# Optimization experiments

Hardware: AMD Instinct MI355X
Metric: run time of the kernel (lower is better)

## Reference

```python
import jax, jax.numpy as jnp
import numpy as np

N = 100000
E = 3200000
IN_C, HID_C, OUT_C = 128, 64, 16
NEG_SLOPE = 0.2


def setup_inputs() -> dict:
    key = jax.random.key(0)
    ks = jax.random.split(key, 12)
    x = jax.random.normal(ks[0], (N, IN_C), dtype=jnp.float32)
    # edges with no self-loops (reference then appends one self-loop per node,
    # matching add_remaining_self_loops on a loop-free graph)
    src = jax.random.randint(ks[1], (E,), 0, N)
    off = jax.random.randint(ks[2], (E,), 1, N)
    dst = (src + off) % N
    edge_index = jnp.stack([src, dst]).astype(jnp.int64)
    W1 = jax.random.normal(ks[3], (IN_C, HID_C), jnp.float32) / np.sqrt(IN_C)
    a_src1 = jax.random.normal(ks[4], (HID_C,), jnp.float32) / np.sqrt(HID_C)
    a_dst1 = jax.random.normal(ks[5], (HID_C,), jnp.float32) / np.sqrt(HID_C)
    b1 = jnp.zeros((HID_C,), jnp.float32)
    W2 = jax.random.normal(ks[6], (HID_C, OUT_C), jnp.float32) / np.sqrt(HID_C)
    a_src2 = jax.random.normal(ks[7], (OUT_C,), jnp.float32) / np.sqrt(OUT_C)
    a_dst2 = jax.random.normal(ks[8], (OUT_C,), jnp.float32) / np.sqrt(OUT_C)
    b2 = jnp.zeros((OUT_C,), jnp.float32)
    return {"x": x, "edge_index": edge_index, "W1": W1, "a_src1": a_src1,
            "a_dst1": a_dst1, "b1": b1, "W2": W2, "a_src2": a_src2,
            "a_dst2": a_dst2, "b2": b2}


def gat_conv(x, src, dst, W, a_src, a_dst, b):
    # x: [N, Cin] -> h: [N, Cout]
    h = x @ W
    # per-node attention halves, then per-edge score e_ij = LeakyReLU(a_s[src]+a_d[dst])
    s = h @ a_src  # [N]
    d = h @ a_dst  # [N]
    e = jax.nn.leaky_relu(s[src] + d[dst], NEG_SLOPE)  # [E']
    # segment softmax over incoming edges of each destination node
    m = jax.ops.segment_max(e, dst, num_segments=N)
    m = jnp.where(jnp.isfinite(m), m, 0.0)
    p = jnp.exp(e - m[dst])
    z = jax.ops.segment_sum(p, dst, num_segments=N)
    coef = p / (z[dst] + 1e-16)  # [E']
    # scatter-aggregate messages h[src] weighted by attention
    out = jax.ops.segment_sum(coef[:, None] * h[src], dst, num_segments=N)
    return out + b


def reference(x, edge_index, W1, a_src1, a_dst1, b1, W2, a_src2, a_dst2, b2):
    # add_remaining_self_loops: input graph has no self-loops, so append all N
    loop = jnp.arange(N, dtype=edge_index.dtype)
    src = jnp.concatenate([edge_index[0], loop])
    dst = jnp.concatenate([edge_index[1], loop])
    h = gat_conv(x, src, dst, W1, a_src1, a_dst1, b1)
    h = jax.nn.relu(h)  # dropout is identity at eval
    h = gat_conv(h, src, dst, W2, a_src2, a_dst2, b2)
    return jax.nn.log_softmax(h, axis=1)
```

## Files before the change

### kernel.cpp

```cpp
#include <hip/hip_runtime.h>
#include <math.h>

#define NEG 0.2f

__device__ __forceinline__ float leaky(float x){ return x >= 0.f ? x : NEG*x; }

__device__ __forceinline__ unsigned short f2b(float f){
    unsigned u = __float_as_uint(f);
    unsigned r = u + 0x7fffu + ((u >> 16) & 1u);
    return (unsigned short)(r >> 16);
}

__global__ void k_rank(const int* __restrict__ ei, int* __restrict__ cnt,
                       int* __restrict__ rank, int E, int ET){
    int i = blockIdx.x*256 + threadIdx.x;
    if (i >= ET) return;
    int dst = (i < E) ? ei[E + i] : (i - E);
    rank[i] = atomicAdd(&cnt[dst << 4], 1);
}
__global__ void k_scan1(const int* __restrict__ cnt, int* __restrict__ bsum, int n){
    __shared__ int sh[256];
    int b = blockIdx.x, tid = threadIdx.x;
    int start = b*1024, s = 0;
    for (int i = tid; i < 1024; i += 256){ int idx = start+i; s += (idx<n)?cnt[idx<<4]:0; }
    sh[tid]=s; __syncthreads();
    for (int d=128; d>0; d>>=1){ if (tid<d) sh[tid]+=sh[tid+d]; __syncthreads(); }
    if (tid==0) bsum[b]=sh[0];
}
__global__ void k_scan2(int* bsum, int nb){
    if (threadIdx.x==0 && blockIdx.x==0){
        int run=0;
        for (int i=0;i<nb;i++){ int v=bsum[i]; bsum[i]=run; run+=v; }
    }
}
__global__ void k_scan3(const int* __restrict__ cnt, const int* __restrict__ bsum,
                        int* __restrict__ rowptr, int n){
    __shared__ int sh[256];
    int b = blockIdx.x, tid = threadIdx.x;
    int i0 = b*1024 + tid*4;
    int v[4]; int local=0;
    #pragma unroll
    for (int k=0;k<4;k++){ int idx=i0+k; v[k]=(idx<n)?cnt[idx<<4]:0; local+=v[k]; }
    sh[tid]=local; __syncthreads();
    for (int d=1; d<256; d<<=1){
        int t = (tid>=d)? sh[tid-d] : 0;
        __syncthreads();
        sh[tid] += t;
        __syncthreads();
    }
    int off = bsum[b] + sh[tid] - local;
    #pragma unroll
    for (int k=0;k<4;k++){
        int idx = i0+k;
        if (idx < n){
            rowptr[idx]=off; off += v[k];
            if (idx==n-1) rowptr[n]=off;
        }
    }
}

__global__ void k_score(const int* __restrict__ ei, const int* __restrict__ rank,
                        const int* __restrict__ rowptr,
                        const float* __restrict__ s, const float* __restrict__ d,
                        int2* __restrict__ csrp, int E, int ET){
    int i = blockIdx.x*256 + threadIdx.x;
    if (i >= ET) return;
    int src = (i < E) ? ei[i]     : (i - E);
    int dst = (i < E) ? ei[E + i] : (i - E);
    float pv = expf(leaky(s[src] + d[dst]));
    csrp[rowptr[dst] + rank[i]] = make_int2(src, __float_as_int(pv));
}

__global__ __launch_bounds__(256) void g1(const float* __restrict__ x,
        const float* __restrict__ W1, const float* __restrict__ a_src,
        const float* __restrict__ a_dst, unsigned short* __restrict__ h1b,
        float* __restrict__ s1, float* __restrict__ d1, int N)
{
    __shared__ float xsh[64][132];
    __shared__ float wsh[128][64];
    const int tid = threadIdx.x;
    const int rowbase = blockIdx.x * 64;
    #pragma unroll
    for (int i = 0; i < 8; ++i){
        int g = tid + i*256;
        ((float4*)&wsh[0][0])[g] = ((const float4*)W1)[g];
    }
    #pragma unroll
    for (int i = 0; i < 8; ++i){
        int g = tid + i*256;
        int r = g >> 5, c4 = g & 31;
        int grow = rowbase + r;
        float4 v = make_float4(0.f,0.f,0.f,0.f);
        if (grow < N) v = ((const float4*)(x + (size_t)grow*128))[c4];
        *(float4*)&xsh[r][c4*4] = v;
    }
    __syncthreads();
    const int tx = tid & 15, ty = tid >> 4;
    float acc[4][4];
    #pragma unroll
    for (int j=0;j<4;++j){
        #pragma unroll
        for (int c=0;c<4;++c) acc[j][c]=0.f;
    }
    #pragma unroll 4
    for (int k4 = 0; k4 < 32; ++k4){
        float4 xv[4], wv[4];
        #pragma unroll
        for (int j=0;j<4;++j) xv[j] = *(const float4*)&xsh[ty*4+j][k4*4];
        #pragma unroll
        for (int i=0;i<4;++i) wv[i] = *(const float4*)&wsh[k4*4+i][tx*4];
        #pragma unroll
        for (int j=0;j<4;++j){
            float x0=xv[j].x, x1=xv[j].y, x2=xv[j].z, x3=xv[j].w;
            acc[j][0]=fmaf(x0,wv[0].x,acc[j][0]); acc[j][1]=fmaf(x0,wv[0].y,acc[j][1]);
            acc[j][2]=fmaf(x0,wv[0].z,acc[j][2]); acc[j][3]=fmaf(x0,wv[0].w,acc[j][3]);
            acc[j][0]=fmaf(x1,wv[1].x,acc[j][0]); acc[j][1]=fmaf(x1,wv[1].y,acc[j][1]);
            acc[j][2]=fmaf(x1,wv[1].z,acc[j][2]); acc[j][3]=fmaf(x1,wv[1].w,acc[j][3]);
            acc[j][0]=fmaf(x2,wv[2].x,acc[j][0]); acc[j][1]=fmaf(x2,wv[2].y,acc[j][1]);
            acc[j][2]=fmaf(x2,wv[2].z,acc[j][2]); acc[j][3]=fmaf(x2,wv[2].w,acc[j][3]);
            acc[j][0]=fmaf(x3,wv[3].x,acc[j][0]); acc[j][1]=fmaf(x3,wv[3].y,acc[j][1]);
            acc[j][2]=fmaf(x3,wv[3].z,acc[j][2]); acc[j][3]=fmaf(x3,wv[3].w,acc[j][3]);
        }
    }
    const float4 asv = *(const float4*)&a_src[tx*4];
    const float4 adv = *(const float4*)&a_dst[tx*4];
    #pragma unroll
    for (int j=0;j<4;++j){
        int r = rowbase + ty*4 + j;
        float sv = acc[j][0]*asv.x + acc[j][1]*asv.y + acc[j][2]*asv.z + acc[j][3]*asv.w;
        float dv = acc[j][0]*adv.x + acc[j][1]*adv.y + acc[j][2]*adv.z + acc[j][3]*adv.w;
        #pragma unroll
        for (int dd=8; dd>0; dd>>=1){ sv += __shfl_xor(sv, dd, 16); dv += __shfl_xor(dv, dd, 16); }
        if (r < N){
            uint2 pk;
            pk.x = (unsigned)f2b(acc[j][0]) | ((unsigned)f2b(acc[j][1]) << 16);
            pk.y = (unsigned)f2b(acc[j][2]) | ((unsigned)f2b(acc[j][3]) << 16);
            *(uint2*)&h1b[(size_t)r*64 + tx*4] = pk;
            if (tx == 0){ s1[r] = sv; d1[r] = dv; }
        }
    }
}

__global__ __launch_bounds__(256) void a1(const int* __restrict__ rowptr,
        const int2* __restrict__ csrp, const unsigned short* __restrict__ h1b,
        const float* __restrict__ b1, float* __restrict__ out1, int N)
{
    int wid = threadIdx.x>>6, lane = threadIdx.x&63;
    int n = blockIdx.x*4 + wid;
    if (n >= N) return;
    int base = rowptr[n], end = rowptr[n+1];
    int es = lane >> 3, cg = lane & 7;
    float a0=0.f,a1v=0.f,a2v=0.f,a3=0.f,a4=0.f,a5=0.f,a6=0.f,a7=0.f;
    float z = 0.f;
    for (int k = base + es; k < end; k += 8){
        int2 cp = csrp[k];
        float pv = __int_as_float(cp.y);
        z += pv;
        uint4 hv = *(const uint4*)(h1b + (size_t)cp.x*64 + cg*8);
        a0 = fmaf(pv, __uint_as_float(hv.x << 16),          a0);
        a1v= fmaf(pv, __uint_as_float(hv.x & 0xffff0000u),  a1v);
        a2v= fmaf(pv, __uint_as_float(hv.y << 16),          a2v);
        a3 = fmaf(pv, __uint_as_float(hv.y & 0xffff0000u),  a3);
        a4 = fmaf(pv, __uint_as_float(hv.z << 16),          a4);
        a5 = fmaf(pv, __uint_as_float(hv.z & 0xffff0000u),  a5);
        a6 = fmaf(pv, __uint_as_float(hv.w << 16),          a6);
        a7 = fmaf(pv, __uint_as_float(hv.w & 0xffff0000u),  a7);
    }
    #pragma unroll
    for (int m = 8; m <= 32; m <<= 1){
        a0 += __shfl_xor(a0, m); a1v += __shfl_xor(a1v, m);
        a2v += __shfl_xor(a2v, m); a3 += __shfl_xor(a3, m);
        a4 += __shfl_xor(a4, m); a5 += __shfl_xor(a5, m);
        a6 += __shfl_xor(a6, m); a7 += __shfl_xor(a7, m);
        z  += __shfl_xor(z, m);
    }
    if (es == 0){
        float zi = 1.f/(z + 1e-16f);
        const float4 b0 = *(const float4*)(b1 + cg*8);
        const float4 b4 = *(const float4*)(b1 + cg*8 + 4);
        float4 o0 = make_float4(fmaxf(a0*zi + b0.x, 0.f), fmaxf(a1v*zi + b0.y, 0.f),
                                fmaxf(a2v*zi + b0.z, 0.f), fmaxf(a3*zi + b0.w, 0.f));
        float4 o4 = make_float4(fmaxf(a4*zi + b4.x, 0.f), fmaxf(a5*zi + b4.y, 0.f),
                                fmaxf(a6*zi + b4.z, 0.f), fmaxf(a7*zi + b4.w, 0.f));
        float* op = out1 + (size_t)n*64 + cg*8;
        *(float4*)op = o0;
        *(float4*)(op+4) = o4;
    }
}

__global__ __launch_bounds__(256) void g2(const float* __restrict__ xin,
        const float* __restrict__ W2, const float* __restrict__ a_src,
        const float* __restrict__ a_dst, unsigned short* __restrict__ h2b,
        float* __restrict__ s2, float* __restrict__ d2, int N)
{
    __shared__ float w[64*16];
    const int tid = threadIdx.x;
    for (int k = tid; k < 64*16/4; k += 256)
        ((float4*)w)[k] = ((const float4*)W2)[k];
    __syncthreads();
    int idx = blockIdx.x*256 + tid;
    int n = idx >> 4, c = idx & 15;
    if (n >= N) return;
    const float as = a_src[c], ad = a_dst[c];
    const float4* xr = (const float4*)(xin + (size_t)n*64);
    float acc = 0.f;
    #pragma unroll
    for (int i4 = 0; i4 < 16; ++i4) {
        float4 v = xr[i4];
        acc = fmaf(v.x, w[(i4*4+0)*16 + c], acc);
        acc = fmaf(v.y, w[(i4*4+1)*16 + c], acc);
        acc = fmaf(v.z, w[(i4*4+2)*16 + c], acc);
        acc = fmaf(v.w, w[(i4*4+3)*16 + c], acc);
    }
    h2b[(size_t)n*16 + c] = f2b(acc);
    float sv = acc*as, dv = acc*ad;
    #pragma unroll
    for (int dd = 8; dd > 0; dd >>= 1){ sv += __shfl_xor(sv, dd, 16); dv += __shfl_xor(dv, dd, 16); }
    if (c == 0) { s2[n] = sv; d2[n] = dv; }
}

__global__ __launch_bounds__(256) void a2(const int* __restrict__ rowptr,
        const int2* __restrict__ csrp, const unsigned short* __restrict__ h2b,
        const float* __restrict__ b2, float* __restrict__ out, int N)
{
    int wid = threadIdx.x>>6, lane = threadIdx.x&63;
    int n = blockIdx.x*4 + wid;
    if (n >= N) return;
    int base = rowptr[n], end = rowptr[n+1];
    int es = lane >> 3, cg = lane & 7;
    float a0=0.f, a1v=0.f, z=0.f;
    for (int k = base + es; k < end; k += 8){
        int2 cp = csrp[k];
        float pv = __int_as_float(cp.y);
        z += pv;
        unsigned hv = *(const unsigned*)(h2b + (size_t)cp.x*16 + cg*2);
        a0 = fmaf(pv, __uint_as_float(hv << 16),         a0);
        a1v= fmaf(pv, __uint_as_float(hv & 0xffff0000u), a1v);
    }
    #pragma unroll
    for (int m = 8; m <= 32; m <<= 1){
        a0 += __shfl_xor(a0, m); a1v += __shfl_xor(a1v, m); z += __shfl_xor(z, m);
    }
    float zi = 1.f/(z + 1e-16f);
    float2 bv = *(const float2*)(b2 + cg*2);
    float o0 = a0*zi + bv.x;
    float o1 = a1v*zi + bv.y;
    float mx = fmaxf(o0, o1);
    #pragma unroll
    for (int m = 1; m <= 4; m <<= 1) mx = fmaxf(mx, __shfl_xor(mx, m));
    float sum = expf(o0 - mx) + expf(o1 - mx);
    #pragma unroll
    for (int m = 1; m <= 4; m <<= 1) sum += __shfl_xor(sum, m);
    if (es == 0){
        float ls = logf(sum);
        *(float2*)(out + (size_t)n*16 + cg*2) = make_float2(o0 - mx - ls, o1 - mx - ls);
    }
}

extern "C" void kernel_launch(void* const* d_in, const int* in_sizes, int n_in,
                              void* d_out, int out_size, void* d_ws, size_t ws_size,
                              hipStream_t stream)
{
    const float* x      = (const float*)d_in[0];
    const int*   ei     = (const int*)d_in[1];
    const float* W1     = (const float*)d_in[2];
    const float* a_src1 = (const float*)d_in[3];
    const float* a_dst1 = (const float*)d_in[4];
    const float* b1     = (const float*)d_in[5];
    const float* W2     = (const float*)d_in[6];
    const float* a_src2 = (const float*)d_in[7];
    const float* a_dst2 = (const float*)d_in[8];
    const float* b2     = (const float*)d_in[9];
    float* out = (float*)d_out;
    const int N  = in_sizes[0] / 128;
    const int E  = in_sizes[1] / 2;
    const int ET = E + N;

    char* ptr = (char*)d_ws;
    auto alloc = [&](size_t bytes)->char* {
        char* r = ptr; ptr += (bytes + 255) & ~(size_t)255; return r;
    };
    unsigned short* h1b    = (unsigned short*)alloc((size_t)N*64*2);
    unsigned short* h2b    = (unsigned short*)alloc((size_t)N*16*2);
    float*          out1   = (float*)alloc((size_t)N*64*4);
    float*          s1     = (float*)alloc((size_t)N*4);
    float*          d1     = (float*)alloc((size_t)N*4);
    float*          s2     = (float*)alloc((size_t)N*4);
    float*          d2v    = (float*)alloc((size_t)N*4);
    int*            cnt    = (int*)alloc((size_t)N*16*4);
    int*            rowptr = (int*)alloc((size_t)(N+1)*4);
    int*            rank   = (int*)alloc((size_t)ET*4);
    int2*           csrp   = (int2*)alloc((size_t)ET*8);
    int*            bsum   = (int*)alloc(4096);

    const int gET  = (ET + 255)/256;
    const int nb1  = (N + 1023)/1024;
    const int nbN4 = (N + 3)/4;
    const int gN16 = ((size_t)N*16 + 255)/256;
    const int gG1  = (N + 63)/64;

    hipMemsetAsync(cnt, 0, (size_t)N*16*4, stream);
    k_rank<<<gET, 256, 0, stream>>>(ei, cnt, rank, E, ET);
    k_scan1<<<nb1, 256, 0, stream>>>(cnt, bsum, N);
    k_scan2<<<1, 64, 0, stream>>>(bsum, nb1);
    k_scan3<<<nb1, 256, 0, stream>>>(cnt, bsum, rowptr, N);

    g1<<<gG1, 256, 0, stream>>>(x, W1, a_src1, a_dst1, h1b, s1, d1, N);
    k_score<<<gET, 256, 0, stream>>>(ei, rank, rowptr, s1, d1, csrp, E, ET);
    a1<<<nbN4, 256, 0, stream>>>(rowptr, csrp, h1b, b1, out1, N);

    g2<<<gN16, 256, 0, stream>>>(out1, W2, a_src2, a_dst2, h2b, s2, d2v, N);
    k_score<<<gET, 256, 0, stream>>>(ei, rank, rowptr, s2, d2v, csrp, E, ET);
    a2<<<nbN4, 256, 0, stream>>>(rowptr, csrp, h2b, b2, out, N);
}
```

Measured before the change: 445.5 us.

## Vectorize edge ranking, compact degree counters, and widen layer-2 aggregation loads

k_rank now handles four edges per thread, with a single int4 load of destinations and an int4 store of ranks. The degree counter array drops its 16-int padding per node and becomes dense, which shrinks the memset and the scan reads. The layer-2 aggregation kernel now gives each edge two lanes that each load 8 bf16 channels with one 16-byte load, so a wave covers 32 edges per iteration instead of 8. The risks are more atomic contention on shared cache lines from the dense counters, and a tail path that could index past N when ET is not a multiple of 4.

After: 448.6 us. No clear change (+0.7%).

```diff
diff --git a/kernel.cpp b/kernel.cpp
--- a/kernel.cpp
+++ b/kernel.cpp
@@ -13,16 +13,30 @@
 
 __global__ void k_rank(const int* __restrict__ ei, int* __restrict__ cnt,
                        int* __restrict__ rank, int E, int ET){
-    int i = blockIdx.x*256 + threadIdx.x;
-    if (i >= ET) return;
-    int dst = (i < E) ? ei[E + i] : (i - E);
-    rank[i] = atomicAdd(&cnt[dst << 4], 1);
+    int i0 = (blockIdx.x*256 + threadIdx.x)*4;
+    if (i0 >= ET) return;
+    int4 r;
+    if (i0 + 3 < E){
+        int4 d4 = *(const int4*)(ei + E + i0);
+        r.x = atomicAdd(&cnt[d4.x], 1);
+        r.y = atomicAdd(&cnt[d4.y], 1);
+        r.z = atomicAdd(&cnt[d4.z], 1);
+        r.w = atomicAdd(&cnt[d4.w], 1);
+    } else {
+        #pragma unroll
+        for (int u = 0; u < 4; ++u){
+            int i = i0 + u;
+            int dst = (i < E) ? ei[E + i] : (i - E);
+            ((int*)&r)[u] = atomicAdd(&cnt[dst], 1);
+        }
+    }
+    *(int4*)(rank + i0) = r;
 }
 __global__ void k_scan1(const int* __restrict__ cnt, int* __restrict__ bsum, int n){
     __shared__ int sh[256];
     int b = blockIdx.x, tid = threadIdx.x;
     int start = b*1024, s = 0;
-    for (int i = tid; i < 1024; i += 256){ int idx = start+i; s += (idx<n)?cnt[idx<<4]:0; }
+    for (int i = tid; i < 1024; i += 256){ int idx = start+i; s += (idx<n)?cnt[idx]:0; }
     sh[tid]=s; __syncthreads();
     for (int d=128; d>0; d>>=1){ if (tid<d) sh[tid]+=sh[tid+d]; __syncthreads(); }
     if (tid==0) bsum[b]=sh[0];
@@ -40,7 +54,7 @@
     int i0 = b*1024 + tid*4;
     int v[4]; int local=0;
     #pragma unroll
-    for (int k=0;k<4;k++){ int idx=i0+k; v[k]=(idx<n)?cnt[idx<<4]:0; local+=v[k]; }
+    for (int k=0;k<4;k++){ int idx=i0+k; v[k]=(idx<n)?cnt[idx]:0; local+=v[k]; }
     sh[tid]=local; __syncthreads();
     for (int d=1; d<256; d<<=1){
         int t = (tid>=d)? sh[tid-d] : 0;
@@ -227,33 +241,48 @@
     int n = blockIdx.x*4 + wid;
     if (n >= N) return;
     int base = rowptr[n], end = rowptr[n+1];
-    int es = lane >> 3, cg = lane & 7;
-    float a0=0.f, a1v=0.f, z=0.f;
-    for (int k = base + es; k < end; k += 8){
+    int es = lane >> 1, cg = lane & 1;
+    float a[8] = {0.f,0.f,0.f,0.f,0.f,0.f,0.f,0.f};
+    float z = 0.f;
+    for (int k = base + es; k < end; k += 32){
         int2 cp = csrp[k];
         float pv = __int_as_float(cp.y);
         z += pv;
-        unsigned hv = *(const unsigned*)(h2b + (size_t)cp.x*16 + cg*2);
-        a0 = fmaf(pv, __uint_as_float(hv << 16),         a0);
-        a1v= fmaf(pv, __uint_as_float(hv & 0xffff0000u), a1v);
-    }
-    #pragma unroll
-    for (int m = 8; m <= 32; m <<= 1){
-        a0 += __shfl_xor(a0, m); a1v += __shfl_xor(a1v, m); z += __shfl_xor(z, m);
+        uint4 hv = *(const uint4*)(h2b + (size_t)cp.x*16 + cg*8);
+        a[0] = fmaf(pv, __uint_as_float(hv.x << 16),          a[0]);
+        a[1] = fmaf(pv, __uint_as_float(hv.x & 0xffff0000u),  a[1]);
+        a[2] = fmaf(pv, __uint_as_float(hv.y << 16),          a[2]);
+        a[3] = fmaf(pv, __uint_as_float(hv.y & 0xffff0000u),  a[3]);
+        a[4] = fmaf(pv, __uint_as_float(hv.z << 16),          a[4]);
+        a[5] = fmaf(pv, __uint_as_float(hv.z & 0xffff0000u),  a[5]);
+        a[6] = fmaf(pv, __uint_as_float(hv.w << 16),          a[6]);
+        a[7] = fmaf(pv, __uint_as_float(hv.w & 0xffff0000u),  a[7]);
+    }
+    #pragma unroll
+    for (int m = 2; m <= 32; m <<= 1){
+        #pragma unroll
+        for (int j = 0; j < 8; ++j) a[j] += __shfl_xor(a[j], m);
+        z += __shfl_xor(z, m);
     }
     float zi = 1.f/(z + 1e-16f);
-    float2 bv = *(const float2*)(b2 + cg*2);
-    float o0 = a0*zi + bv.x;
-    float o1 = a1v*zi + bv.y;
-    float mx = fmaxf(o0, o1);
-    #pragma unroll
-    for (int m = 1; m <= 4; m <<= 1) mx = fmaxf(mx, __shfl_xor(mx, m));
-    float sum = expf(o0 - mx) + expf(o1 - mx);
-    #pragma unroll
-    for (int m = 1; m <= 4; m <<= 1) sum += __shfl_xor(sum, m);
+    const float4 b0 = *(const float4*)(b2 + cg*8);
+    const float4 b4 = *(const float4*)(b2 + cg*8 + 4);
+    float o[8];
+    o[0]=a[0]*zi+b0.x; o[1]=a[1]*zi+b0.y; o[2]=a[2]*zi+b0.z; o[3]=a[3]*zi+b0.w;
+    o[4]=a[4]*zi+b4.x; o[5]=a[5]*zi+b4.y; o[6]=a[6]*zi+b4.z; o[7]=a[7]*zi+b4.w;
+    float mx = o[0];
+    #pragma unroll
+    for (int j = 1; j < 8; ++j) mx = fmaxf(mx, o[j]);
+    mx = fmaxf(mx, __shfl_xor(mx, 1));
+    float sum = 0.f;
+    #pragma unroll
+    for (int j = 0; j < 8; ++j) sum += expf(o[j] - mx);
+    sum += __shfl_xor(sum, 1);
     if (es == 0){
         float ls = logf(sum);
-        *(float2*)(out + (size_t)n*16 + cg*2) = make_float2(o0 - mx - ls, o1 - mx - ls);
+        float* op = out + (size_t)n*16 + cg*8;
+        *(float4*)op     = make_float4(o[0]-mx-ls, o[1]-mx-ls, o[2]-mx-ls, o[3]-mx-ls);
+        *(float4*)(op+4) = make_float4(o[4]-mx-ls, o[5]-mx-ls, o[6]-mx-ls, o[7]-mx-ls);
     }
 }
 
@@ -287,20 +316,21 @@
     float*          d1     = (float*)alloc((size_t)N*4);
     float*          s2     = (float*)alloc((size_t)N*4);
     float*          d2v    = (float*)alloc((size_t)N*4);
-    int*            cnt    = (int*)alloc((size_t)N*16*4);
+    int*            cnt    = (int*)alloc((size_t)N*4);
     int*            rowptr = (int*)alloc((size_t)(N+1)*4);
-    int*            rank   = (int*)alloc((size_t)ET*4);
+    int*            rank   = (int*)alloc((size_t)(ET+3)*4);
     int2*           csrp   = (int2*)alloc((size_t)ET*8);
     int*            bsum   = (int*)alloc(4096);
 
     const int gET  = (ET + 255)/256;
+    const int gET4 = ((ET+3)/4 + 255)/256;
     const int nb1  = (N + 1023)/1024;
     const int nbN4 = (N + 3)/4;
     const int gN16 = ((size_t)N*16 + 255)/256;
     const int gG1  = (N + 63)/64;
 
-    hipMemsetAsync(cnt, 0, (size_t)N*16*4, stream);
-    k_rank<<<gET, 256, 0, stream>>>(ei, cnt, rank, E, ET);
+    hipMemsetAsync(cnt, 0, (size_t)N*4, stream);
+    k_rank<<<gET4, 256, 0, stream>>>(ei, cnt, rank, E, ET);
     k_scan1<<<nb1, 256, 0, stream>>>(cnt, bsum, N);
     k_scan2<<<1, 64, 0, stream>>>(bsum, nb1);
     k_scan3<<<nb1, 256, 0, stream>>>(cnt, bsum, rowptr, N);
```
